# Kernel tuning notes

Measured on AMD Instinct MI355X. Metric: run time of the kernel, lower is better.

The kernel has to match this reference:

```python
import jax, jax.numpy as jnp
import numpy as np

B, H, E, V, T = 8, 1024, 512, 32000, 100


def setup_inputs() -> dict:
    key = jax.random.key(0)
    ks = jax.random.split(key, 6)
    output = jax.random.normal(ks[0], (1, B, H), jnp.float32)       # decoder GRU output [seq=1, B, H]
    input_step = jax.random.normal(ks[1], (1, B, E), jnp.float32)   # embedded input token
    context = jax.random.normal(ks[2], (1, B, H), jnp.float32)      # attention context
    topic_indexs = jax.random.randint(ks[3], (B, T), 0, V)          # topic word ids (0 = pad)
    W_V = jax.random.normal(ks[4], (V, H + E), jnp.float32) / np.sqrt(H + E)
    b_V = jnp.zeros((V,), jnp.float32)
    W_K = jax.random.normal(ks[5], (V, 2 * H + E), jnp.float32) / np.sqrt(2 * H + E)
    b_K = jnp.zeros((V,), jnp.float32)
    return {
        "output": output, "input_step": input_step, "context": context,
        "topic_indexs": topic_indexs, "topic_length": T,
        "W_V": W_V, "b_V": b_V, "W_K": W_K, "b_K": b_K,
    }


def _topic_counts(topic_indexs, vocab, dtype):
    # Faithful to one_hot_embedding (identity with row 0 zeroed) summed over dim=1:
    # k[b, w] = #{t : topic_indexs[b, t] == w}, with index 0 contributing nothing.
    b = topic_indexs.shape[0]
    k = jnp.zeros((b, vocab), dtype).at[jnp.arange(b)[:, None], topic_indexs].add(1.0)
    return k.at[:, 0].set(0.0)


def reference(output, input_step, context, topic_indexs, topic_length, W_V, b_V, W_K, b_K):
    vocab = W_V.shape[0]
    k = _topic_counts(topic_indexs, vocab, output.dtype)            # [B, V]
    v = (k == 0).astype(output.dtype)                               # [B, V]
    x_v = jnp.concatenate([output, input_step], axis=2)             # [1, B, H+E]
    x_k = jnp.concatenate([output, input_step, context], axis=2)    # [1, B, 2H+E]
    e_v = x_v @ W_V.T + b_V                                         # [1, B, V]
    e_k = x_k @ W_K.T + b_K                                         # [1, B, V]
    energy = jnp.tanh(v * e_v + k * e_k)                            # [1, B, V] (k,v broadcast)
    prob = jax.nn.softmax(energy, axis=-1)
    return prob.squeeze()                                           # [B, V]
```

## Files before the change

### kernel.cpp

```cpp
#include <hip/hip_runtime.h>
#include <hip/hip_bf16.h>

#define BB 8
#define HH 1024
#define EE 512
#define VV 32000
#define TT 100
#define KV 1536
#define KK 2560

__global__ __launch_bounds__(256) void ev_kernel(
    const float* __restrict__ output, const float* __restrict__ input_step,
    const float* __restrict__ W_V, const float* __restrict__ b_V,
    float* __restrict__ d_out, float* __restrict__ blocksums) {
  __shared__ float xv[BB * KV];
  __shared__ float wavesums[4][8];

  const int tid = threadIdx.x;

  for (int i = tid; i < BB * KV / 4; i += 256) {
    int b = i / (KV / 4);
    int pos = (i - b * (KV / 4)) * 4;
    float4 v;
    if (pos < HH) v = *(const float4*)(output + b * HH + pos);
    else          v = *(const float4*)(input_step + b * EE + (pos - HH));
    *(float4*)(xv + b * KV + pos) = v;
  }
  __syncthreads();

  const int wave = tid >> 6;
  const int lane = tid & 63;
  const int w0 = blockIdx.x * 16 + wave * 4;

  float acc[4][8];
#pragma unroll
  for (int r = 0; r < 4; ++r)
#pragma unroll
    for (int b = 0; b < 8; ++b) acc[r][b] = 0.f;

#pragma unroll 2
  for (int jg = 0; jg < 6; ++jg) {
    const int jb = jg * 256 + lane * 4;
    float4 wv0 = *(const float4*)(W_V + (size_t)(w0 + 0) * KV + jb);
    float4 wv1 = *(const float4*)(W_V + (size_t)(w0 + 1) * KV + jb);
    float4 wv2 = *(const float4*)(W_V + (size_t)(w0 + 2) * KV + jb);
    float4 wv3 = *(const float4*)(W_V + (size_t)(w0 + 3) * KV + jb);
#pragma unroll
    for (int b = 0; b < 8; ++b) {
      float4 x = *(const float4*)(xv + b * KV + jb);
      acc[0][b] += wv0.x * x.x + wv0.y * x.y + wv0.z * x.z + wv0.w * x.w;
      acc[1][b] += wv1.x * x.x + wv1.y * x.y + wv1.z * x.z + wv1.w * x.w;
      acc[2][b] += wv2.x * x.x + wv2.y * x.y + wv2.z * x.z + wv2.w * x.w;
      acc[3][b] += wv3.x * x.x + wv3.y * x.y + wv3.z * x.z + wv3.w * x.w;
    }
  }

  float myval = 0.f;
#pragma unroll
  for (int r = 0; r < 4; ++r) {
#pragma unroll
    for (int b = 0; b < 8; ++b) {
      float v = acc[r][b];
#pragma unroll
      for (int off = 32; off; off >>= 1) v += __shfl_xor(v, off, 64);
      if (lane == r * 8 + b) myval = v;
    }
  }

  float p = 0.f;
  if (lane < 32) {
    const int r = lane >> 3;
    const int b = lane & 7;
    const int w = w0 + r;
    float ev = myval + b_V[w];
    p = expf(tanhf(ev));
    d_out[(size_t)b * VV + w] = p;
  }
  p += __shfl_xor(p, 8, 64);
  p += __shfl_xor(p, 16, 64);
  p += __shfl_xor(p, 32, 64);
  if (lane < 8) wavesums[wave][lane] = p;
  __syncthreads();
  if (tid < 8) {
    float s = wavesums[0][tid] + wavesums[1][tid] + wavesums[2][tid] + wavesums[3][tid];
    blocksums[(size_t)blockIdx.x * 8 + tid] = s;
  }
}

__global__ __launch_bounds__(256) void topic_kernel(
    const float* __restrict__ output, const float* __restrict__ input_step,
    const float* __restrict__ context, const int* __restrict__ topic_idx,
    const float* __restrict__ W_K, const float* __restrict__ b_K,
    float* __restrict__ d_out, float* __restrict__ topic_delta) {
  const int wave = threadIdx.x >> 6;
  const int lane = threadIdx.x & 63;
  const int task = blockIdx.x * 4 + wave;
  const int b = task / TT;
  const int t = task - b * TT;
  const int w = topic_idx[b * TT + t];

  bool valid = (w != 0);
  int k = 0, first = TT;
  if (valid) {
    for (int t2 = 0; t2 < TT; ++t2) {
      int w2 = topic_idx[b * TT + t2];
      if (w2 == w) { ++k; if (t2 < first) first = t2; }
    }
    valid = (first == t);
  }
  if (!valid) {
    if (lane == 0) topic_delta[task] = 0.f;
    return;
  }

  float s = 0.f;
#pragma unroll
  for (int i = 0; i < 10; ++i) {
    const int j = i * 256 + lane * 4;
    float4 wk = *(const float4*)(W_K + (size_t)w * KK + j);
    const float* xs;
    if (j < HH)            xs = output + b * HH + j;
    else if (j < HH + EE)  xs = input_step + b * EE + (j - HH);
    else                   xs = context + b * HH + (j - HH - EE);
    float4 x = *(const float4*)xs;
    s += wk.x * x.x + wk.y * x.y + wk.z * x.z + wk.w * x.w;
  }
#pragma unroll
  for (int off = 32; off; off >>= 1) s += __shfl_xor(s, off, 64);

  float ek = s + b_K[w];
  float p = expf(tanhf((float)k * ek));
  if (lane == 0) {
    float pold = d_out[(size_t)b * VV + w];
    d_out[(size_t)b * VV + w] = p;
    topic_delta[task] = p - pold;
  }
}

__global__ __launch_bounds__(256) void reduce_kernel(
    const float* __restrict__ blocksums, const float* __restrict__ topic_delta,
    float* __restrict__ sums, int nblocks) {
  const int b = blockIdx.x;
  const int tid = threadIdx.x;
  float s = 0.f;
  for (int i = tid; i < nblocks; i += 256) s += blocksums[(size_t)i * 8 + b];
  if (tid < TT) s += topic_delta[b * TT + tid];
  __shared__ float red[4];
#pragma unroll
  for (int off = 32; off; off >>= 1) s += __shfl_xor(s, off, 64);
  if ((tid & 63) == 0) red[tid >> 6] = s;
  __syncthreads();
  if (tid == 0) sums[b] = red[0] + red[1] + red[2] + red[3];
}

__global__ __launch_bounds__(256) void norm_kernel(
    float* __restrict__ d_out, const float* __restrict__ sums) {
  const int i = blockIdx.x * 256 + threadIdx.x;
  const int b = i / (VV / 4);
  float4 v = *((const float4*)d_out + i);
  const float s = sums[b];
  v.x /= s; v.y /= s; v.z /= s; v.w /= s;
  *((float4*)d_out + i) = v;
}

extern "C" void kernel_launch(void* const* d_in, const int* in_sizes, int n_in,
                              void* d_out, int out_size, void* d_ws, size_t ws_size,
                              hipStream_t stream) {
  const float* output     = (const float*)d_in[0];
  const float* input_step = (const float*)d_in[1];
  const float* context    = (const float*)d_in[2];
  const int*   topic_idx  = (const int*)d_in[3];
  const float* W_V = (const float*)d_in[5];
  const float* b_V = (const float*)d_in[6];
  const float* W_K = (const float*)d_in[7];
  const float* b_K = (const float*)d_in[8];
  float* out = (float*)d_out;

  float* ws_f        = (float*)d_ws;
  float* topic_delta = ws_f;
  float* blocksums   = ws_f + 800;
  float* sums        = ws_f + 800 + 16000;

  const int nblocks = VV / 16;

  ev_kernel<<<nblocks, 256, 0, stream>>>(output, input_step, W_V, b_V, out, blocksums);
  topic_kernel<<<(BB * TT) / 4, 256, 0, stream>>>(output, input_step, context,
                                                  topic_idx, W_K, b_K, out, topic_delta);
  reduce_kernel<<<BB, 256, 0, stream>>>(blocksums, topic_delta, sums, nblocks);
  norm_kernel<<<(VV / 4) * BB / 256, 256, 0, stream>>>(out, sums);
}
```

Measured before the change: 510.8 us.

## Drop LDS staging of activations and use transpose-style butterfly reduction in ev_kernel

The ev_kernel no longer copies the 8x1536 activation tile into shared memory. It reads the activations directly from global memory, where they will largely hit in cache, which removes a 48KB LDS allocation and a block barrier and should allow higher occupancy. The 32 per-lane accumulators are now reduced with a recursive-halving shuffle butterfly, about 32 shuffles instead of 192, and a bit-permuted lane index maps each result back to its row and batch. The topic kernel spreads its duplicate-count scan across lanes with shuffle reductions, and the dot products use explicit fmaf chains. The trade-off is more global and L2 activation loads per block.

After: 533.0 us. 1.04x slower.

```diff
diff --git a/kernel.cpp b/kernel.cpp
--- a/kernel.cpp
+++ b/kernel.cpp
@@ -13,77 +13,72 @@
     const float* __restrict__ output, const float* __restrict__ input_step,
     const float* __restrict__ W_V, const float* __restrict__ b_V,
     float* __restrict__ d_out, float* __restrict__ blocksums) {
-  __shared__ float xv[BB * KV];
   __shared__ float wavesums[4][8];
 
   const int tid = threadIdx.x;
-
-  for (int i = tid; i < BB * KV / 4; i += 256) {
-    int b = i / (KV / 4);
-    int pos = (i - b * (KV / 4)) * 4;
-    float4 v;
-    if (pos < HH) v = *(const float4*)(output + b * HH + pos);
-    else          v = *(const float4*)(input_step + b * EE + (pos - HH));
-    *(float4*)(xv + b * KV + pos) = v;
-  }
-  __syncthreads();
-
   const int wave = tid >> 6;
   const int lane = tid & 63;
   const int w0 = blockIdx.x * 16 + wave * 4;
 
-  float acc[4][8];
+  float v[32];
 #pragma unroll
-  for (int r = 0; r < 4; ++r)
-#pragma unroll
-    for (int b = 0; b < 8; ++b) acc[r][b] = 0.f;
+  for (int i = 0; i < 32; ++i) v[i] = 0.f;
 
 #pragma unroll 2
   for (int jg = 0; jg < 6; ++jg) {
-    const int jb = jg * 256 + lane * 4;
-    float4 wv0 = *(const float4*)(W_V + (size_t)(w0 + 0) * KV + jb);
-    float4 wv1 = *(const float4*)(W_V + (size_t)(w0 + 1) * KV + jb);
-    float4 wv2 = *(const float4*)(W_V + (size_t)(w0 + 2) * KV + jb);
-    float4 wv3 = *(const float4*)(W_V + (size_t)(w0 + 3) * KV + jb);
+    const int off = jg * 256 + lane * 4;
+    float4 wv0 = *(const float4*)(W_V + (size_t)(w0 + 0) * KV + off);
+    float4 wv1 = *(const float4*)(W_V + (size_t)(w0 + 1) * KV + off);
+    float4 wv2 = *(const float4*)(W_V + (size_t)(w0 + 2) * KV + off);
+    float4 wv3 = *(const float4*)(W_V + (size_t)(w0 + 3) * KV + off);
+    const float* xb;
+    int stride;
+    if (jg < 4) { xb = output + off;          stride = HH; }
+    else        { xb = input_step + off - HH; stride = EE; }
 #pragma unroll
     for (int b = 0; b < 8; ++b) {
-      float4 x = *(const float4*)(xv + b * KV + jb);
-      acc[0][b] += wv0.x * x.x + wv0.y * x.y + wv0.z * x.z + wv0.w * x.w;
-      acc[1][b] += wv1.x * x.x + wv1.y * x.y + wv1.z * x.z + wv1.w * x.w;
-      acc[2][b] += wv2.x * x.x + wv2.y * x.y + wv2.z * x.z + wv2.w * x.w;
-      acc[3][b] += wv3.x * x.x + wv3.y * x.y + wv3.z * x.z + wv3.w * x.w;
+      float4 x = *(const float4*)(xb + b * stride);
+      v[0 * 8 + b] = fmaf(wv0.w, x.w, fmaf(wv0.z, x.z, fmaf(wv0.y, x.y, fmaf(wv0.x, x.x, v[0 * 8 + b]))));
+      v[1 * 8 + b] = fmaf(wv1.w, x.w, fmaf(wv1.z, x.z, fmaf(wv1.y, x.y, fmaf(wv1.x, x.x, v[1 * 8 + b]))));
+      v[2 * 8 + b] = fmaf(wv2.w, x.w, fmaf(wv2.z, x.z, fmaf(wv2.y, x.y, fmaf(wv2.x, x.x, v[2 * 8 + b]))));
+      v[3 * 8 + b] = fmaf(wv3.w, x.w, fmaf(wv3.z, x.z, fmaf(wv3.y, x.y, fmaf(wv3.x, x.x, v[3 * 8 + b]))));
     }
   }
 
-  float myval = 0.f;
 #pragma unroll
-  for (int r = 0; r < 4; ++r) {
+  for (int step = 0; step < 5; ++step) {
+    const int m = 1 << step;
+    const int half = 16 >> step;
+    const bool upper = (lane & m) != 0;
 #pragma unroll
-    for (int b = 0; b < 8; ++b) {
-      float v = acc[r][b];
-#pragma unroll
-      for (int off = 32; off; off >>= 1) v += __shfl_xor(v, off, 64);
-      if (lane == r * 8 + b) myval = v;
+    for (int i = 0; i < half; ++i) {
+      float send = upper ? v[i] : v[i + half];
+      float keep = upper ? v[i + half] : v[i];
+      v[i] = keep + __shfl_xor(send, m, 64);
     }
   }
+  v[0] += __shfl_xor(v[0], 32, 64);
 
+  const int j = ((lane & 1) << 4) | ((lane & 2) << 2) | (lane & 4) |
+                ((lane & 8) >> 2) | ((lane & 16) >> 4);
   float p = 0.f;
   if (lane < 32) {
-    const int r = lane >> 3;
-    const int b = lane & 7;
+    const int r = j >> 3;
+    const int b = j & 7;
     const int w = w0 + r;
-    float ev = myval + b_V[w];
+    float ev = v[0] + b_V[w];
     p = expf(tanhf(ev));
     d_out[(size_t)b * VV + w] = p;
   }
-  p += __shfl_xor(p, 8, 64);
-  p += __shfl_xor(p, 16, 64);
-  p += __shfl_xor(p, 32, 64);
-  if (lane < 8) wavesums[wave][lane] = p;
+  p += __shfl_xor(p, 1, 64);
+  p += __shfl_xor(p, 2, 64);
+  if ((lane & 35) == 0) {
+    wavesums[wave][j & 7] = p;
+  }
   __syncthreads();
   if (tid < 8) {
-    float s = wavesums[0][tid] + wavesums[1][tid] + wavesums[2][tid] + wavesums[3][tid];
-    blocksums[(size_t)blockIdx.x * 8 + tid] = s;
+    blocksums[(size_t)blockIdx.x * 8 + tid] =
+        wavesums[0][tid] + wavesums[1][tid] + wavesums[2][tid] + wavesums[3][tid];
   }
 }
 
@@ -99,15 +94,17 @@
   const int t = task - b * TT;
   const int w = topic_idx[b * TT + t];
 
-  bool valid = (w != 0);
   int k = 0, first = TT;
-  if (valid) {
-    for (int t2 = 0; t2 < TT; ++t2) {
-      int w2 = topic_idx[b * TT + t2];
-      if (w2 == w) { ++k; if (t2 < first) first = t2; }
-    }
-    valid = (first == t);
+  for (int t2 = lane; t2 < TT; t2 += 64) {
+    int w2 = topic_idx[b * TT + t2];
+    if (w2 == w) { ++k; first = min(first, t2); }
   }
+#pragma unroll
+  for (int off = 32; off; off >>= 1) {
+    k += __shfl_xor(k, off, 64);
+    first = min(first, __shfl_xor(first, off, 64));
+  }
+  const bool valid = (w != 0) && (first == t);
   if (!valid) {
     if (lane == 0) topic_delta[task] = 0.f;
     return;
@@ -123,14 +120,13 @@
     else if (j < HH + EE)  xs = input_step + b * EE + (j - HH);
     else                   xs = context + b * HH + (j - HH - EE);
     float4 x = *(const float4*)xs;
-    s += wk.x * x.x + wk.y * x.y + wk.z * x.z + wk.w * x.w;
+    s = fmaf(wk.w, x.w, fmaf(wk.z, x.z, fmaf(wk.y, x.y, fmaf(wk.x, x.x, s))));
   }
 #pragma unroll
   for (int off = 32; off; off >>= 1) s += __shfl_xor(s, off, 64);
 
-  float ek = s + b_K[w];
-  float p = expf(tanhf((float)k * ek));
   if (lane == 0) {
+    float p = expf(tanhf((float)k * (s + b_K[w])));
     float pold = d_out[(size_t)b * VV + w];
     d_out[(size_t)b * VV + w] = p;
     topic_delta[task] = p - pold;
```
